# Performance work log

Measured on AMD Instinct MI355X. Metric: run time of the kernel, lower is better.

## Reference

```python
import jax, jax.numpy as jnp
import numpy as np

B, T, N, H, P = 16, 64, 512, 128, 12


def _laplacian_with_self_loop(adj):
    a = adj + jnp.eye(adj.shape[0], dtype=adj.dtype)
    d_inv_sqrt = 1.0 / jnp.sqrt(a.sum(axis=1))
    return a * d_inv_sqrt[:, None] * d_inv_sqrt[None, :]


def setup_inputs() -> dict:
    key = jax.random.key(0)
    ks = jax.random.split(key, 10)
    inputs = jax.random.normal(ks[0], (B, T, N), dtype=jnp.float32)
    adj = jax.random.uniform(ks[1], (N, N), dtype=jnp.float32)
    adj = (adj + adj.T) * 0.5
    laplacian = _laplacian_with_self_loop(adj)

    def xavier(k, shape):
        fan_in, fan_out = shape[0], shape[1]
        lim = np.sqrt(6.0 / (fan_in + fan_out))
        return jax.random.uniform(k, shape, jnp.float32, -lim, lim)

    W1 = xavier(ks[2], (H + 1, 2 * H))      # graph_conv1 weights
    b1 = jnp.ones((2 * H,), jnp.float32)    # bias init 1.0
    W2 = xavier(ks[3], (H + 1, H))          # graph_conv2 weights
    b2 = jnp.zeros((H,), jnp.float32)
    att_w1 = xavier(ks[4], (H, 1))
    att_w2 = xavier(ks[5], (N, 1))
    att_w3 = xavier(ks[6], (N, 1))
    att_b1 = jnp.zeros((1,), jnp.float32)
    att_b2 = jnp.zeros((1,), jnp.float32)
    att_b3 = jnp.zeros((1,), jnp.float32)
    W_out = xavier(ks[7], (T, P))
    b_out = jnp.zeros((P,), jnp.float32)
    return dict(inputs=inputs, laplacian=laplacian, W1=W1, b1=b1, W2=W2, b2=b2,
                att_w1=att_w1, att_w2=att_w2, att_w3=att_w3,
                att_b1=att_b1, att_b2=att_b2, att_b3=att_b3,
                W_out=W_out, b_out=b_out)


def reference(inputs, laplacian, W1, b1, W2, b2,
              att_w1, att_w2, att_w3, att_b1, att_b2, att_b3,
              W_out, b_out):
    Bs, Ts, Ns = inputs.shape
    Hs = W2.shape[1]

    def graph_conv(x_t, h_flat, W, b):
        # x_t: [B,N]; h_flat: [B, N*H]
        h = h_flat.reshape(Bs, Ns, Hs)
        conc = jnp.concatenate([x_t[..., None], h], axis=-1)     # [B,N,H+1]
        agg = jnp.einsum('mn,bnc->bmc', laplacian, conc)          # [B,N,H+1]
        out = agg @ W + b                                         # [B,N,O]
        return out.reshape(Bs, -1)                                # [B,N*O] (flattened, matching torch)

    def step(h_flat, x_t):
        ru = jax.nn.sigmoid(graph_conv(x_t, h_flat, W1, b1))      # [B, N*2H]
        r, u = jnp.split(ru, 2, axis=1)                            # split on flattened dim (faithful)
        c = jnp.tanh(graph_conv(x_t, r * h_flat, W2, b2))          # [B, N*H]
        new_h = u * h_flat + (1.0 - u) * c
        return new_h, new_h

    h0 = jnp.zeros((Bs, Ns * Hs), inputs.dtype)
    _, hs = jax.lax.scan(step, h0, jnp.moveaxis(inputs, 1, 0))     # [T,B,N*H]
    hidden_states = jnp.moveaxis(hs, 0, 1).reshape(Bs, Ts, Ns, Hs)

    # SelfAttention: project H->1, then N->1 per (b,t), softmax over T
    hs1 = hidden_states.reshape(-1, Hs) @ att_w1 + att_b1          # [B*T*N, 1]
    f = (hs1.reshape(-1, Ns) @ att_w2 + att_b2).reshape(Bs, Ts)
    g = (hs1.reshape(-1, Ns) @ att_w3 + att_b3).reshape(Bs, Ts)
    beta = jax.nn.softmax(g * f, axis=-1)                          # [B,T]
    context = beta[:, :, None] * hs1.reshape(Bs, Ts, Ns)           # [B,T,N]

    context = context.transpose(0, 2, 1)                           # [B,N,T]
    Ps = W_out.shape[1]
    out = (context.reshape(-1, Ts) @ W_out + b_out).reshape(Bs, Ns, Ps)
    return out.transpose(0, 2, 1)                                  # [B,pre_len,N]
```

## Files before the change

### kernel.cpp

```cpp
#include <hip/hip_runtime.h>
#include <math.h>

#define B_ 16
#define T_ 64
#define N_ 512
#define H_ 128
#define P_ 12
#define NH 65536

__global__ __launch_bounds__(512) void lx_kernel(const float* __restrict__ x,
                                                 const float* __restrict__ L,
                                                 float* __restrict__ Lx) {
    __shared__ __align__(16) float xs[2][N_];
    const int r0 = blockIdx.x * 2;
    const int tid = threadIdx.x;
    for (int j = 0; j < 2; ++j)
        xs[j][tid] = x[(size_t)(r0 + j) * N_ + tid];
    __syncthreads();
    float a0 = 0.f, a1 = 0.f;
    const int m = tid;
#pragma unroll 8
    for (int n = 0; n < N_; ++n) {
        float lv = L[(size_t)n * N_ + m];
        a0 += xs[0][n] * lv;
        a1 += xs[1][n] * lv;
    }
    Lx[(size_t)(r0 + 0) * N_ + m] = a0;
    Lx[(size_t)(r0 + 1) * N_ + m] = a1;
}

#define FMA4(dst, a, hv)                                                      \
    dst[0] += (a) * (hv).x; dst[1] += (a) * (hv).y;                           \
    dst[2] += (a) * (hv).z; dst[3] += (a) * (hv).w;

__global__ __launch_bounds__(512) void gc1_kernel(
    const float* __restrict__ L, const float* __restrict__ Hprev,
    const float* __restrict__ Lx, const float* __restrict__ W1,
    const float* __restrict__ b1, float* __restrict__ rh,
    float* __restrict__ u, int t) {
    __shared__ __align__(16) float Ht[2][32][H_];
    union LW {
        float Lt[2][32][20];
        float Wt[16][260];
    };
    __shared__ __align__(16) LW sm;
    __shared__ __align__(16) float Zb[16][H_];

    const int tid = threadIdx.x;
    const int b = blockIdx.x & 15;
    const int m0 = (blockIdx.x >> 4) * 16;
    const float* __restrict__ Hb = Hprev + (size_t)b * NH;

    const int hrow = tid >> 5, hcol = (tid & 31) * 4;
    const int lm = tid >> 5, lk = tid & 31;

    {
        *(float4*)&Ht[0][hrow][hcol] = *(const float4*)&Hb[(size_t)hrow * H_ + hcol];
        *(float4*)&Ht[0][hrow + 16][hcol] =
            *(const float4*)&Hb[(size_t)(hrow + 16) * H_ + hcol];
        sm.Lt[0][lk][lm] = L[(size_t)(m0 + lm) * N_ + lk];
    }
    __syncthreads();

    const int g = tid >> 6;
    const int l = tid & 63;
    const int ty = l >> 4;
    const int tx = l & 15;
    const int ma0 = ty * 4;
    const int ca0 = tx * 4, cb0 = 64 + tx * 4;

    float acc[4][2][4] = {};

    for (int kc = 0; kc < 16; ++kc) {
        const int bi = kc & 1, bj = bi ^ 1;
        float4 p0, p1;
        float pl;
        if (kc < 15) {
            const size_t kb = (size_t)(kc + 1) * 32;
            p0 = *(const float4*)&Hb[(kb + hrow) * H_ + hcol];
            p1 = *(const float4*)&Hb[(kb + hrow + 16) * H_ + hcol];
            pl = L[(size_t)(m0 + lm) * N_ + kb + lk];
        }
#pragma unroll
        for (int kk = 0; kk < 4; ++kk) {
            const int k = g * 4 + kk;
            const float4 la = *(const float4*)&sm.Lt[bi][k][ma0];
            const float4 h0 = *(const float4*)&Ht[bi][k][ca0];
            const float4 h1 = *(const float4*)&Ht[bi][k][cb0];
            FMA4(acc[0][0], la.x, h0) FMA4(acc[0][1], la.x, h1)
            FMA4(acc[1][0], la.y, h0) FMA4(acc[1][1], la.y, h1)
            FMA4(acc[2][0], la.z, h0) FMA4(acc[2][1], la.z, h1)
            FMA4(acc[3][0], la.w, h0) FMA4(acc[3][1], la.w, h1)
        }
        if (kc < 15) {
            *(float4*)&Ht[bj][hrow][hcol] = p0;
            *(float4*)&Ht[bj][hrow + 16][hcol] = p1;
            sm.Lt[bj][lk][lm] = pl;
        }
        __syncthreads();
    }

    for (int r = 0; r < 8; ++r) {
        if (g == r) {
#pragma unroll
            for (int i = 0; i < 4; ++i) {
#pragma unroll
                for (int v = 0; v < 2; ++v) {
                    const int c = v ? cb0 : ca0;
                    float4* zp = (float4*)&Zb[ma0 + i][c];
                    if (r == 0) {
                        *zp = make_float4(acc[i][v][0], acc[i][v][1],
                                          acc[i][v][2], acc[i][v][3]);
                    } else {
                        float4 z = *zp;
                        *zp = make_float4(z.x + acc[i][v][0], z.y + acc[i][v][1],
                                          z.z + acc[i][v][2], z.w + acc[i][v][3]);
                    }
                }
            }
        }
        __syncthreads();
    }

    const int to = tid & 63, tm = tid >> 6;
    const int o0 = to * 4;
    float a2[2][4] = {};
    const int wr = tid >> 5, wc = (tid & 31) * 4;

    for (int ck = 0; ck < 8; ++ck) {
        *(float4*)&sm.Wt[wr][wc] =
            *(const float4*)&W1[(size_t)(1 + ck * 16 + wr) * 256 + wc];
        *(float4*)&sm.Wt[wr][wc + 128] =
            *(const float4*)&W1[(size_t)(1 + ck * 16 + wr) * 256 + wc + 128];
        __syncthreads();
#pragma unroll
        for (int ch4 = 0; ch4 < 4; ++ch4) {
            const float4 w0v = *(const float4*)&sm.Wt[ch4 * 4 + 0][o0];
            const float4 w1v = *(const float4*)&sm.Wt[ch4 * 4 + 1][o0];
            const float4 w2v = *(const float4*)&sm.Wt[ch4 * 4 + 2][o0];
            const float4 w3v = *(const float4*)&sm.Wt[ch4 * 4 + 3][o0];
            const int cc = ck * 16 + ch4 * 4;
#pragma unroll
            for (int i = 0; i < 2; ++i) {
                const float4 zv = *(const float4*)&Zb[tm + 8 * i][cc];
                a2[i][0] += zv.x * w0v.x + zv.y * w1v.x + zv.z * w2v.x + zv.w * w3v.x;
                a2[i][1] += zv.x * w0v.y + zv.y * w1v.y + zv.z * w2v.y + zv.w * w3v.y;
                a2[i][2] += zv.x * w0v.z + zv.y * w1v.z + zv.z * w2v.z + zv.w * w3v.z;
                a2[i][3] += zv.x * w0v.w + zv.y * w1v.w + zv.z * w2v.w + zv.w * w3v.w;
            }
        }
        __syncthreads();
    }

    const float4 w0r = *(const float4*)&W1[o0];
    const float4 bbv = *(const float4*)&b1[o0];
    const float* __restrict__ LxRow = Lx + ((size_t)b * T_ + t) * N_ + m0;
    float* __restrict__ rhB = rh + (size_t)b * NH;
    float* __restrict__ uB = u + (size_t)b * NH;
    const bool isR = (m0 < 256);
#pragma unroll
    for (int i = 0; i < 2; ++i) {
        const int mi = tm + 8 * i;
        const float lx = LxRow[mi];
        float v0 = a2[i][0] + lx * w0r.x + bbv.x;
        float v1 = a2[i][1] + lx * w0r.y + bbv.y;
        float v2 = a2[i][2] + lx * w0r.z + bbv.z;
        float v3 = a2[i][3] + lx * w0r.w + bbv.w;
        float s0 = 1.f / (1.f + expf(-v0));
        float s1 = 1.f / (1.f + expf(-v1));
        float s2 = 1.f / (1.f + expf(-v2));
        float s3 = 1.f / (1.f + expf(-v3));
        const int fl = (m0 + mi) * 256 + o0;
        if (isR) {
            float4 hv = *(const float4*)&Hb[fl];
            *(float4*)&rhB[fl] = make_float4(s0 * hv.x, s1 * hv.y, s2 * hv.z, s3 * hv.w);
        } else {
            *(float4*)&uB[fl - NH] = make_float4(s0, s1, s2, s3);
        }
    }
}

__global__ __launch_bounds__(256) void y_kernel(
    const float* __restrict__ rh, const float* __restrict__ W2,
    float* __restrict__ Y) {
    __shared__ __align__(16) float Zs[8][H_];
    __shared__ __align__(16) float Wt[16][H_];

    const int tid = threadIdx.x;
    const int b = blockIdx.x & 15;
    const int n0 = (blockIdx.x >> 4) * 8;
    const size_t gbase = (size_t)b * NH + (size_t)n0 * H_;

    const int row = tid >> 5;
    const int o0 = (tid & 31) * 4;

    *(float4*)&Zs[row][o0] = *(const float4*)&rh[gbase + (size_t)row * H_ + o0];

    float a2[4] = {0.f, 0.f, 0.f, 0.f};

#pragma unroll 1
    for (int ck = 0; ck < 8; ++ck) {
        __syncthreads();
        *(float4*)&Wt[row][o0] =
            *(const float4*)&W2[(size_t)(1 + ck * 16 + row) * H_ + o0];
        *(float4*)&Wt[row + 8][o0] =
            *(const float4*)&W2[(size_t)(1 + ck * 16 + row + 8) * H_ + o0];
        __syncthreads();
#pragma unroll
        for (int ch4 = 0; ch4 < 4; ++ch4) {
            const float4 w0v = *(const float4*)&Wt[ch4 * 4 + 0][o0];
            const float4 w1v = *(const float4*)&Wt[ch4 * 4 + 1][o0];
            const float4 w2v = *(const float4*)&Wt[ch4 * 4 + 2][o0];
            const float4 w3v = *(const float4*)&Wt[ch4 * 4 + 3][o0];
            const float4 zv = *(const float4*)&Zs[row][ck * 16 + ch4 * 4];
            a2[0] += zv.x * w0v.x + zv.y * w1v.x + zv.z * w2v.x + zv.w * w3v.x;
            a2[1] += zv.x * w0v.y + zv.y * w1v.y + zv.z * w2v.y + zv.w * w3v.y;
            a2[2] += zv.x * w0v.z + zv.y * w1v.z + zv.z * w2v.z + zv.w * w3v.z;
            a2[3] += zv.x * w0v.w + zv.y * w1v.w + zv.z * w2v.w + zv.w * w3v.w;
        }
    }

    *(float4*)&Y[gbase + (size_t)row * H_ + o0] =
        make_float4(a2[0], a2[1], a2[2], a2[3]);
}

__global__ __launch_bounds__(512) void gcz_kernel(
    const float* __restrict__ L, const float* __restrict__ Y,
    const float* __restrict__ Hprev, const float* __restrict__ u,
    const float* __restrict__ Lx, const float* __restrict__ W2,
    const float* __restrict__ b2, const float* __restrict__ aw1,
    const float* __restrict__ ab1, float* __restrict__ Hnew,
    float* __restrict__ hs1, int t) {
    __shared__ __align__(16) float Ht[2][32][H_];
    __shared__ __align__(16) float Lt[2][32][20];
    __shared__ __align__(16) float Zb[16][H_];
    __shared__ __align__(16) float pad_[2880];

    const int tid = threadIdx.x;
    if (tid < 16) pad_[tid] = 0.f;
    asm volatile("" ::: "memory");

    const int b = blockIdx.x & 15;
    const int m0 = (blockIdx.x >> 4) * 16;
    const float* __restrict__ Yb = Y + (size_t)b * NH;

    const int hrow = tid >> 5, hcol = (tid & 31) * 4;
    const int lm = tid >> 5, lk = tid & 31;

    {
        *(float4*)&Ht[0][hrow][hcol] = *(const float4*)&Yb[(size_t)hrow * H_ + hcol];
        *(float4*)&Ht[0][hrow + 16][hcol] =
            *(const float4*)&Yb[(size_t)(hrow + 16) * H_ + hcol];
        Lt[0][lk][lm] = L[(size_t)(m0 + lm) * N_ + lk];
    }
    __syncthreads();

    const int g = tid >> 6;
    const int l = tid & 63;
    const int ty = l >> 4;
    const int tx = l & 15;
    const int ma0 = ty * 4;
    const int ca0 = tx * 4, cb0 = 64 + tx * 4;

    float acc[4][2][4] = {};

    for (int kc = 0; kc < 16; ++kc) {
        const int bi = kc & 1, bj = bi ^ 1;
        float4 p0, p1;
        float pl;
        if (kc < 15) {
            const size_t kb = (size_t)(kc + 1) * 32;
            p0 = *(const float4*)&Yb[(kb + hrow) * H_ + hcol];
            p1 = *(const float4*)&Yb[(kb + hrow + 16) * H_ + hcol];
            pl = L[(size_t)(m0 + lm) * N_ + kb + lk];
        }
#pragma unroll
        for (int kk = 0; kk < 4; ++kk) {
            const int k = g * 4 + kk;
            const float4 la = *(const float4*)&Lt[bi][k][ma0];
            const float4 h0 = *(const float4*)&Ht[bi][k][ca0];
            const float4 h1 = *(const float4*)&Ht[bi][k][cb0];
            FMA4(acc[0][0], la.x, h0) FMA4(acc[0][1], la.x, h1)
            FMA4(acc[1][0], la.y, h0) FMA4(acc[1][1], la.y, h1)
            FMA4(acc[2][0], la.z, h0) FMA4(acc[2][1], la.z, h1)
            FMA4(acc[3][0], la.w, h0) FMA4(acc[3][1], la.w, h1)
        }
        if (kc < 15) {
            *(float4*)&Ht[bj][hrow][hcol] = p0;
            *(float4*)&Ht[bj][hrow + 16][hcol] = p1;
            Lt[bj][lk][lm] = pl;
        }
        __syncthreads();
    }

    for (int r = 0; r < 8; ++r) {
        if (g == r) {
#pragma unroll
            for (int i = 0; i < 4; ++i) {
#pragma unroll
                for (int v = 0; v < 2; ++v) {
                    const int c = v ? cb0 : ca0;
                    float4* zp = (float4*)&Zb[ma0 + i][c];
                    if (r == 0) {
                        *zp = make_float4(acc[i][v][0], acc[i][v][1],
                                          acc[i][v][2], acc[i][v][3]);
                    } else {
                        float4 z = *zp;
                        *zp = make_float4(z.x + acc[i][v][0], z.y + acc[i][v][1],
                                          z.z + acc[i][v][2], z.w + acc[i][v][3]);
                    }
                }
            }
        }
        __syncthreads();
    }

    const int zr = tid >> 5;
    const int zc = (tid & 31) * 4;
    const float4 zv = *(const float4*)&Zb[zr][zc];
    const float4 w0r = *(const float4*)&W2[zc];
    const float4 bbv = *(const float4*)&b2[zc];
    const float4 awv = *(const float4*)&aw1[zc];
    const float lx = Lx[((size_t)b * T_ + t) * N_ + m0 + zr];

    float c0 = tanhf(zv.x + lx * w0r.x + bbv.x);
    float c1 = tanhf(zv.y + lx * w0r.y + bbv.y);
    float c2 = tanhf(zv.z + lx * w0r.z + bbv.z);
    float c3 = tanhf(zv.w + lx * w0r.w + bbv.w);

    const size_t fl = (size_t)b * NH + (size_t)(m0 + zr) * H_ + zc;
    const float4 uv = *(const float4*)&u[fl];
    const float4 hp = *(const float4*)&Hprev[fl];
    const float h0 = uv.x * hp.x + (1.f - uv.x) * c0;
    const float h1 = uv.y * hp.y + (1.f - uv.y) * c1;
    const float h2 = uv.z * hp.z + (1.f - uv.z) * c2;
    const float h3 = uv.w * hp.w + (1.f - uv.w) * c3;
    *(float4*)&Hnew[fl] = make_float4(h0, h1, h2, h3);

    float part = h0 * awv.x + h1 * awv.y + h2 * awv.z + h3 * awv.w;
#pragma unroll
    for (int off = 16; off; off >>= 1) part += __shfl_xor(part, off);
    if ((tid & 31) == 0)
        hs1[((size_t)b * T_ + t) * N_ + m0 + zr] = part + ab1[0];
}

__global__ __launch_bounds__(64) void att_beta_kernel(
    const float* __restrict__ hs1, const float* __restrict__ aw2,
    const float* __restrict__ aw3, const float* __restrict__ ab2,
    const float* __restrict__ ab3, float* __restrict__ beta) {
    const int b = blockIdx.x;
    const int t = threadIdx.x;
    const float* __restrict__ row = hs1 + ((size_t)b * T_ + t) * N_;
    float f = 0.f, g = 0.f;
    for (int n = 0; n < N_; n += 4) {
        float4 hv = *(const float4*)&row[n];
        float4 w2v = *(const float4*)&aw2[n];
        float4 w3v = *(const float4*)&aw3[n];
        f += hv.x * w2v.x + hv.y * w2v.y + hv.z * w2v.z + hv.w * w2v.w;
        g += hv.x * w3v.x + hv.y * w3v.y + hv.z * w3v.z + hv.w * w3v.w;
    }
    f += ab2[0];
    g += ab3[0];
    float s = f * g;
    float mx = s;
    for (int off = 32; off; off >>= 1) mx = fmaxf(mx, __shfl_xor(mx, off));
    float e = expf(s - mx);
    float sum = e;
    for (int off = 32; off; off >>= 1) sum += __shfl_xor(sum, off);
    beta[b * T_ + t] = e / sum;
}

__global__ __launch_bounds__(256) void att_out_kernel(
    const float* __restrict__ hs1, const float* __restrict__ beta,
    const float* __restrict__ Wout, const float* __restrict__ bout,
    float* __restrict__ out) {
    __shared__ float bs[T_];
    __shared__ float ws[T_][P_];
    const int b = blockIdx.x;
    const int tid = threadIdx.x;
    if (tid < T_) bs[tid] = beta[b * T_ + tid];
    for (int i = tid; i < T_ * P_; i += 256) ws[i / P_][i % P_] = Wout[i];
    __syncthreads();
    for (int nn = 0; nn < 2; ++nn) {
        const int n = tid + nn * 256;
        float acc[P_];
#pragma unroll
        for (int p = 0; p < P_; ++p) acc[p] = bout[p];
        for (int t = 0; t < T_; ++t) {
            float v = bs[t] * hs1[((size_t)b * T_ + t) * N_ + n];
#pragma unroll
            for (int p = 0; p < P_; ++p) acc[p] += v * ws[t][p];
        }
#pragma unroll
        for (int p = 0; p < P_; ++p) out[((size_t)b * P_ + p) * N_ + n] = acc[p];
    }
}

extern "C" void kernel_launch(void* const* d_in, const int* in_sizes, int n_in,
                              void* d_out, int out_size, void* d_ws, size_t ws_size,
                              hipStream_t stream) {
    const float* x = (const float*)d_in[0];
    const float* L = (const float*)d_in[1];
    const float* W1 = (const float*)d_in[2];
    const float* b1 = (const float*)d_in[3];
    const float* W2 = (const float*)d_in[4];
    const float* b2 = (const float*)d_in[5];
    const float* aw1 = (const float*)d_in[6];
    const float* aw2 = (const float*)d_in[7];
    const float* aw3 = (const float*)d_in[8];
    const float* ab1 = (const float*)d_in[9];
    const float* ab2 = (const float*)d_in[10];
    const float* ab3 = (const float*)d_in[11];
    const float* Wout = (const float*)d_in[12];
    const float* bout = (const float*)d_in[13];
    float* out = (float*)d_out;

    float* ws = (float*)d_ws;
    float* Lx = ws;
    float* hs1 = Lx + B_ * T_ * N_;
    float* hb0 = hs1 + B_ * T_ * N_;
    float* hb1 = hb0 + (size_t)B_ * NH;
    float* rh = hb1 + (size_t)B_ * NH;
    float* u = rh + (size_t)B_ * NH;
    float* Ybuf = u + (size_t)B_ * NH;
    float* beta = Ybuf + (size_t)B_ * NH;
    (void)in_sizes; (void)n_in; (void)out_size; (void)ws_size;

    hipMemsetAsync(hb0, 0, (size_t)B_ * NH * sizeof(float), stream);
    lx_kernel<<<512, 512, 0, stream>>>(x, L, Lx);

    for (int t = 0; t < T_; ++t) {
        float* hp = (t & 1) ? hb1 : hb0;
        float* hn = (t & 1) ? hb0 : hb1;
        gc1_kernel<<<512, 512, 0, stream>>>(L, hp, Lx, W1, b1, rh, u, t);
        y_kernel<<<1024, 256, 0, stream>>>(rh, W2, Ybuf);
        gcz_kernel<<<512, 512, 0, stream>>>(L, Ybuf, hp, u, Lx, W2, b2, aw1,
                                            ab1, hn, hs1, t);
    }
    att_beta_kernel<<<16, 64, 0, stream>>>(hs1, aw2, aw3, ab2, ab3, beta);
    att_out_kernel<<<16, 256, 0, stream>>>(hs1, beta, Wout, bout, out);
}
```

Before: 4.154 ms.

## Fuse r*h times W2 projection into gc1 kernel via LDS staging

The r-gate blocks of the first graph-conv kernel now keep r*h in LDS and multiply it by W2 directly, writing Y without a separate y_kernel launch or the rh round trip through global memory. This removes one launch per timestep and a full-size write and read of rh. In exchange it adds 16KB of LDS per block, which may lower occupancy, and leaves the work unbalanced: only the r-half blocks do the extra GEMM while the u-half blocks finish early.

Result: faster. 3.656 ms (-12.0%).

```diff
diff --git a/kernel.cpp b/kernel.cpp
--- a/kernel.cpp
+++ b/kernel.cpp
@@ -33,11 +33,11 @@
     dst[0] += (a) * (hv).x; dst[1] += (a) * (hv).y;                           \
     dst[2] += (a) * (hv).z; dst[3] += (a) * (hv).w;
 
-__global__ __launch_bounds__(512) void gc1_kernel(
+__global__ __launch_bounds__(512) void gc1y_kernel(
     const float* __restrict__ L, const float* __restrict__ Hprev,
     const float* __restrict__ Lx, const float* __restrict__ W1,
-    const float* __restrict__ b1, float* __restrict__ rh,
-    float* __restrict__ u, int t) {
+    const float* __restrict__ b1, const float* __restrict__ W2,
+    float* __restrict__ Y, float* __restrict__ u, int t) {
     __shared__ __align__(16) float Ht[2][32][H_];
     union LW {
         float Lt[2][32][20];
@@ -45,6 +45,7 @@
     };
     __shared__ __align__(16) LW sm;
     __shared__ __align__(16) float Zb[16][H_];
+    __shared__ __align__(16) float R_lds[32][H_];
 
     const int tid = threadIdx.x;
     const int b = blockIdx.x & 15;
@@ -155,73 +156,78 @@
     const float4 w0r = *(const float4*)&W1[o0];
     const float4 bbv = *(const float4*)&b1[o0];
     const float* __restrict__ LxRow = Lx + ((size_t)b * T_ + t) * N_ + m0;
-    float* __restrict__ rhB = rh + (size_t)b * NH;
-    float* __restrict__ uB = u + (size_t)b * NH;
     const bool isR = (m0 < 256);
-#pragma unroll
-    for (int i = 0; i < 2; ++i) {
-        const int mi = tm + 8 * i;
-        const float lx = LxRow[mi];
-        float v0 = a2[i][0] + lx * w0r.x + bbv.x;
-        float v1 = a2[i][1] + lx * w0r.y + bbv.y;
-        float v2 = a2[i][2] + lx * w0r.z + bbv.z;
-        float v3 = a2[i][3] + lx * w0r.w + bbv.w;
-        float s0 = 1.f / (1.f + expf(-v0));
-        float s1 = 1.f / (1.f + expf(-v1));
-        float s2 = 1.f / (1.f + expf(-v2));
-        float s3 = 1.f / (1.f + expf(-v3));
-        const int fl = (m0 + mi) * 256 + o0;
-        if (isR) {
+
+    if (isR) {
+#pragma unroll
+        for (int i = 0; i < 2; ++i) {
+            const int mi = tm + 8 * i;
+            const float lx = LxRow[mi];
+            float v0 = a2[i][0] + lx * w0r.x + bbv.x;
+            float v1 = a2[i][1] + lx * w0r.y + bbv.y;
+            float v2 = a2[i][2] + lx * w0r.z + bbv.z;
+            float v3 = a2[i][3] + lx * w0r.w + bbv.w;
+            float s0 = 1.f / (1.f + expf(-v0));
+            float s1 = 1.f / (1.f + expf(-v1));
+            float s2 = 1.f / (1.f + expf(-v2));
+            float s3 = 1.f / (1.f + expf(-v3));
+            const int fl = (m0 + mi) * 256 + o0;
             float4 hv = *(const float4*)&Hb[fl];
-            *(float4*)&rhB[fl] = make_float4(s0 * hv.x, s1 * hv.y, s2 * hv.z, s3 * hv.w);
-        } else {
+            const int rr2 = 2 * mi + (o0 >> 7);
+            *(float4*)&R_lds[rr2][o0 & 127] =
+                make_float4(s0 * hv.x, s1 * hv.y, s2 * hv.z, s3 * hv.w);
+        }
+        __syncthreads();
+
+        const int rr = tid >> 5;
+        const int oc = (tid & 31) * 4;
+        float a3[2][4] = {};
+        for (int ck = 0; ck < 8; ++ck) {
+            *(float4*)&sm.Wt[wr][wc] =
+                *(const float4*)&W2[(size_t)(1 + ck * 16 + wr) * H_ + wc];
+            __syncthreads();
+#pragma unroll
+            for (int ch4 = 0; ch4 < 4; ++ch4) {
+                const float4 w0v = *(const float4*)&sm.Wt[ch4 * 4 + 0][oc];
+                const float4 w1v = *(const float4*)&sm.Wt[ch4 * 4 + 1][oc];
+                const float4 w2v = *(const float4*)&sm.Wt[ch4 * 4 + 2][oc];
+                const float4 w3v = *(const float4*)&sm.Wt[ch4 * 4 + 3][oc];
+                const int cc = ck * 16 + ch4 * 4;
+#pragma unroll
+                for (int i = 0; i < 2; ++i) {
+                    const float4 zv = *(const float4*)&R_lds[rr + 16 * i][cc];
+                    a3[i][0] += zv.x * w0v.x + zv.y * w1v.x + zv.z * w2v.x + zv.w * w3v.x;
+                    a3[i][1] += zv.x * w0v.y + zv.y * w1v.y + zv.z * w2v.y + zv.w * w3v.y;
+                    a3[i][2] += zv.x * w0v.z + zv.y * w1v.z + zv.z * w2v.z + zv.w * w3v.z;
+                    a3[i][3] += zv.x * w0v.w + zv.y * w1v.w + zv.z * w2v.w + zv.w * w3v.w;
+                }
+            }
+            __syncthreads();
+        }
+        float* __restrict__ Yb = Y + (size_t)b * NH;
+#pragma unroll
+        for (int i = 0; i < 2; ++i) {
+            *(float4*)&Yb[(size_t)(2 * m0 + rr + 16 * i) * H_ + oc] =
+                make_float4(a3[i][0], a3[i][1], a3[i][2], a3[i][3]);
+        }
+    } else {
+        float* __restrict__ uB = u + (size_t)b * NH;
+#pragma unroll
+        for (int i = 0; i < 2; ++i) {
+            const int mi = tm + 8 * i;
+            const float lx = LxRow[mi];
+            float v0 = a2[i][0] + lx * w0r.x + bbv.x;
+            float v1 = a2[i][1] + lx * w0r.y + bbv.y;
+            float v2 = a2[i][2] + lx * w0r.z + bbv.z;
+            float v3 = a2[i][3] + lx * w0r.w + bbv.w;
+            float s0 = 1.f / (1.f + expf(-v0));
+            float s1 = 1.f / (1.f + expf(-v1));
+            float s2 = 1.f / (1.f + expf(-v2));
+            float s3 = 1.f / (1.f + expf(-v3));
+            const int fl = (m0 + mi) * 256 + o0;
             *(float4*)&uB[fl - NH] = make_float4(s0, s1, s2, s3);
         }
     }
-}
-
-__global__ __launch_bounds__(256) void y_kernel(
-    const float* __restrict__ rh, const float* __restrict__ W2,
-    float* __restrict__ Y) {
-    __shared__ __align__(16) float Zs[8][H_];
-    __shared__ __align__(16) float Wt[16][H_];
-
-    const int tid = threadIdx.x;
-    const int b = blockIdx.x & 15;
-    const int n0 = (blockIdx.x >> 4) * 8;
-    const size_t gbase = (size_t)b * NH + (size_t)n0 * H_;
-
-    const int row = tid >> 5;
-    const int o0 = (tid & 31) * 4;
-
-    *(float4*)&Zs[row][o0] = *(const float4*)&rh[gbase + (size_t)row * H_ + o0];
-
-    float a2[4] = {0.f, 0.f, 0.f, 0.f};
-
-#pragma unroll 1
-    for (int ck = 0; ck < 8; ++ck) {
-        __syncthreads();
-        *(float4*)&Wt[row][o0] =
-            *(const float4*)&W2[(size_t)(1 + ck * 16 + row) * H_ + o0];
-        *(float4*)&Wt[row + 8][o0] =
-            *(const float4*)&W2[(size_t)(1 + ck * 16 + row + 8) * H_ + o0];
-        __syncthreads();
-#pragma unroll
-        for (int ch4 = 0; ch4 < 4; ++ch4) {
-            const float4 w0v = *(const float4*)&Wt[ch4 * 4 + 0][o0];
-            const float4 w1v = *(const float4*)&Wt[ch4 * 4 + 1][o0];
-            const float4 w2v = *(const float4*)&Wt[ch4 * 4 + 2][o0];
-            const float4 w3v = *(const float4*)&Wt[ch4 * 4 + 3][o0];
-            const float4 zv = *(const float4*)&Zs[row][ck * 16 + ch4 * 4];
-            a2[0] += zv.x * w0v.x + zv.y * w1v.x + zv.z * w2v.x + zv.w * w3v.x;
-            a2[1] += zv.x * w0v.y + zv.y * w1v.y + zv.z * w2v.y + zv.w * w3v.y;
-            a2[2] += zv.x * w0v.z + zv.y * w1v.z + zv.z * w2v.z + zv.w * w3v.z;
-            a2[3] += zv.x * w0v.w + zv.y * w1v.w + zv.z * w2v.w + zv.w * w3v.w;
-        }
-    }
-
-    *(float4*)&Y[gbase + (size_t)row * H_ + o0] =
-        make_float4(a2[0], a2[1], a2[2], a2[3]);
 }
 
 __global__ __launch_bounds__(512) void gcz_kernel(
@@ -420,8 +426,7 @@
     float* hs1 = Lx + B_ * T_ * N_;
     float* hb0 = hs1 + B_ * T_ * N_;
     float* hb1 = hb0 + (size_t)B_ * NH;
-    float* rh = hb1 + (size_t)B_ * NH;
-    float* u = rh + (size_t)B_ * NH;
+    float* u = hb1 + (size_t)B_ * NH;
     float* Ybuf = u + (size_t)B_ * NH;
     float* beta = Ybuf + (size_t)B_ * NH;
     (void)in_sizes; (void)n_in; (void)out_size; (void)ws_size;
@@ -432,8 +437,7 @@
     for (int t = 0; t < T_; ++t) {
         float* hp = (t & 1) ? hb1 : hb0;
         float* hn = (t & 1) ? hb0 : hb1;
-        gc1_kernel<<<512, 512, 0, stream>>>(L, hp, Lx, W1, b1, rh, u, t);
-        y_kernel<<<1024, 256, 0, stream>>>(rh, W2, Ybuf);
+        gc1y_kernel<<<512, 512, 0, stream>>>(L, hp, Lx, W1, b1, W2, Ybuf, u, t);
         gcz_kernel<<<512, 512, 0, stream>>>(L, Ybuf, hp, u, Lx, W2, b2, aw1,
                                             ab1, hn, hs1, t);
     }
```
